# Optimization experiments

Hardware: AMD Instinct MI355X
Metric: run time of the kernel (lower is better)

The kernel has to match this reference:

```python
import jax, jax.numpy as jnp
import numpy as np

D_EMBED = 512
N_HEAD = 8
N_LAYER = 12
B, S = 4, 1024


def setup_inputs() -> dict:
    key = jax.random.key(0)
    ks = jax.random.split(key, 8)
    std = 0.02
    x = jax.random.normal(ks[0], (B, S, D_EMBED), dtype=jnp.float32)
    e = jax.random.normal(ks[1], (B, S, D_EMBED), dtype=jnp.float32)
    p = jax.random.normal(ks[2], (S, D_EMBED), dtype=jnp.float32)
    W_q = std * jax.random.normal(ks[3], (N_HEAD, D_EMBED, D_EMBED), dtype=jnp.float32)
    W_k = std * jax.random.normal(ks[4], (N_HEAD, D_EMBED, D_EMBED), dtype=jnp.float32)
    W_v = std * jax.random.normal(ks[5], (N_HEAD, D_EMBED, D_EMBED), dtype=jnp.float32)
    # torch Linear weight: (out_features, in_features) = (E, H*E)
    W_o = (std / np.sqrt(2 * N_LAYER)) * jax.random.normal(ks[6], (D_EMBED, N_HEAD * D_EMBED), dtype=jnp.float32)
    gamma = std * jax.random.normal(ks[7], (1, N_HEAD, 1, 1), dtype=jnp.float32)
    return {"x": x, "e": e, "p": p, "W_q": W_q, "W_k": W_k, "W_v": W_v, "W_o": W_o, "gamma": gamma}


def reference(x, e, p, W_q, W_k, W_v, W_o, gamma):
    # use_ppe_attn=False path: Q,K,V all from x. Per-head full-dim projections.
    Q = jnp.einsum('bse,hef->bhsf', x, W_q)  # (B,H,S,E)
    K = jnp.einsum('bse,hef->bhsf', x, W_k)
    V = jnp.einsum('bse,hef->bhsf', x, W_v)
    # rbf kernel: exp(-gamma * ||q - k||_2^2), squared distance via expansion
    q2 = jnp.sum(Q * Q, axis=-1, keepdims=True)          # (B,H,S,1)
    k2 = jnp.sum(K * K, axis=-1, keepdims=True)          # (B,H,S,1)
    qk = jnp.einsum('bhse,bhte->bhst', Q, K)             # (B,H,S,S)
    d2 = jnp.maximum(q2 + jnp.swapaxes(k2, -2, -1) - 2.0 * qk, 0.0)
    attn = jnp.exp(-gamma * d2)                          # (B,H,S,S)
    out = jnp.einsum('bhst,bhte->bhse', attn, V)         # (B,H,S,E)
    out = jnp.transpose(out, (0, 2, 1, 3)).reshape(x.shape[0], x.shape[1], -1)  # (B,S,H*E)
    return out @ W_o.T                                   # (B,S,E)
```

## Files before the change

### kernel.cpp

```cpp
#include <hip/hip_runtime.h>
#include <cstdint>
#include <cstring>

typedef unsigned short ushort_t;
typedef __attribute__((ext_vector_type(8))) short short8;
typedef __attribute__((ext_vector_type(4))) float f32x4;
typedef __attribute__((ext_vector_type(4))) unsigned short us4;

constexpr int Hh = 8;
constexpr int Ss = 1024;
constexpr int Ee = 512;

__device__ __forceinline__ ushort_t f2bf(float f) {
    uint32_t u; __builtin_memcpy(&u, &f, 4);
    u += 0x7fffu + ((u >> 16) & 1u);
    return (ushort_t)(u >> 16);
}
__device__ __forceinline__ float bf2f(ushort_t h) {
    uint32_t u = ((uint32_t)h) << 16; float f; __builtin_memcpy(&f, &u, 4); return f;
}

__device__ __forceinline__ void gload_lds16(const ushort_t* g, void* lds) {
    __builtin_amdgcn_global_load_lds(
        (const __attribute__((address_space(1))) void*)g,
        (__attribute__((address_space(3))) void*)lds, 16, 0, 0);
}


__global__ void cvt_f32_bf16(const float4* __restrict__ in, us4* __restrict__ out, int n4) {
    int i = blockIdx.x * blockDim.x + threadIdx.x;
    if (i < n4) {
        float4 v = in[i];
        us4 o = { f2bf(v.x), f2bf(v.y), f2bf(v.z), f2bf(v.w) };
        out[i] = o;
    }
}

__global__ void wtrans(const float* __restrict__ W, ushort_t* __restrict__ Wt) {
    __shared__ float tile[32][33];
    int h = blockIdx.z;
    int e0 = blockIdx.y * 32, f0 = blockIdx.x * 32;
    int tx = threadIdx.x, ty = threadIdx.y;
    #pragma unroll
    for (int i = 0; i < 4; i++) {
        int e = e0 + ty + i * 8;
        tile[ty + i * 8][tx] = W[((size_t)h * 512 + e) * 512 + f0 + tx];
    }
    __syncthreads();
    #pragma unroll
    for (int i = 0; i < 4; i++) {
        int f = f0 + ty + i * 8;
        Wt[((size_t)h * 512 + f) * 512 + e0 + tx] = f2bf(tile[tx][ty + i * 8]);
    }
}

__global__ void sumsq(const ushort_t* __restrict__ X, float* __restrict__ out) {
    int row = blockIdx.x * 4 + (threadIdx.x >> 6);
    int ln = threadIdx.x & 63;
    short8 v = *(const short8*)(X + (size_t)row * 512 + ln * 8);
    float s = 0.f;
    #pragma unroll
    for (int j = 0; j < 8; j++) {
        float f = bf2f((ushort_t)v[j]);
        s += f * f;
    }
    #pragma unroll
    for (int off = 32; off > 0; off >>= 1) s += __shfl_xor(s, off);
    if (ln == 0) out[row] = s;
}

__global__ void reduce8(const f32x4* __restrict__ p, f32x4* __restrict__ out, int n4) {
    int i = blockIdx.x * blockDim.x + threadIdx.x;
    if (i < n4) {
        f32x4 a = __builtin_nontemporal_load(p + i);
        #pragma unroll
        for (int j = 1; j < 8; j++) a += __builtin_nontemporal_load(p + i + (size_t)j * n4);
        out[i] = a;
    }
}

template<int EPI>
__global__ __launch_bounds__(512, 1)
void gemm256(const ushort_t* __restrict__ A, int lda,
             const ushort_t* __restrict__ Bm, int ldb,
             void* __restrict__ Cout, int K,
             const float* __restrict__ q2, const float* __restrict__ k2,
             const float* __restrict__ gamma, int bIdx)
{
    __shared__ __align__(16) ushort_t SMEM[65536];

    const int t  = threadIdx.x;
    const int wv = t >> 6, ln = t & 63;
    const int wm = wv >> 2, wn = wv & 3;

    const int gx = gridDim.x, gy = gridDim.y;
    const int gxy = gx * gy;
    const int L = blockIdx.x + gx * (blockIdx.y + gy * blockIdx.z);
    const int xcd = L & 7;
    const int j = L >> 3;
    const int z  = xcd + 8 * (j / gxy);
    const int rem = j % gxy;
    const int by = rem / gx;
    const int bx = rem % gx;

    const int m0 = by * 256, n0 = bx * 256;

    int bh = z;
    if constexpr (EPI == 2 || EPI == 3) bh = (bIdx < 0) ? z : (bIdx * Hh + z);

    const ushort_t* Ab = A;
    const ushort_t* Bb = Bm;
    if constexpr (EPI == 0 || EPI == 1) { Bb = Bm + (size_t)z * Ee * Ee; }
    if constexpr (EPI == 2) {
        Ab = A  + (size_t)bh * Ss * Ee;
        Bb = Bm + (size_t)bh * Ss * Ee;
    }
    if constexpr (EPI == 3) {
        Ab = A  + (size_t)z * Ss * Ss;
        Bb = Bm + (size_t)bh * Ee * Ss;
    }
    if constexpr (EPI == 4) {
        Ab = A  + (size_t)z * 512;
        Bb = Bm + (size_t)z * 512;
    }

    f32x4 acc[8][4];
    #pragma unroll
    for (int i = 0; i < 8; i++)
        #pragma unroll
        for (int j2 = 0; j2 < 4; j2++) acc[i][j2] = (f32x4){0.f, 0.f, 0.f, 0.f};

    const int srow = ln >> 3;
    const int schk = ((ln & 7) ^ srow) * 8;
    const ushort_t* sbase[4][2];
    int ldso[4][2];
    #pragma unroll
    for (int kind = 0; kind < 4; ++kind) {
        #pragma unroll
        for (int c = 0; c < 2; ++c) {
            const int idx = (kind & 1) * 16 + wv * 2 + c;
            const int rb = idx * 8 + srow;
            sbase[kind][c] = (kind < 2)
                ? Ab + (size_t)(m0 + rb) * lda + schk
                : Bb + (size_t)(n0 + rb) * ldb + schk;
            ldso[kind][c] = (kind < 2 ? 0 : 32768) + idx * 512;
        }
    }
    auto STAGE_UNIT = [&](int tile, int kind) {
        const int k0 = tile << 6;
        const int par = (tile & 1) * 16384;
        #pragma unroll
        for (int c = 0; c < 2; ++c)
            gload_lds16(sbase[kind][c] + k0, &SMEM[ldso[kind][c] + par]);
    };

    const int T = K >> 6;

    #pragma unroll
    for (int kk = 0; kk < 4; ++kk) STAGE_UNIT(0, kk);
    #pragma unroll
    for (int kk = 0; kk < 4; ++kk) STAGE_UNIT(1, kk);
    asm volatile("s_waitcnt vmcnt(8)" ::: "memory");
    __builtin_amdgcn_s_barrier();

    const int lrow = ln & 15, lkg = ln >> 4;
    const int swz = lrow & 7;

    for (int u = 0; u < (T >> 1); ++u) {
        short8 bfr[4][2];
        #pragma unroll
        for (int p = 0; p < 8; ++p) {
            const int d = p >> 2, q = p & 3;

            if (q == 0) {
                #pragma unroll
                for (int fc = 0; fc < 4; fc++)
                    #pragma unroll
                    for (int kg = 0; kg < 2; kg++)
                        bfr[fc][kg] = *(const short8*)(&SMEM[32768 + d * 16384 +
                                          (wn * 64 + fc * 16 + lrow) * 64 +
                                          (((kg * 4 + lkg) ^ swz) << 3)]);
            }
            short8 af[2][2];
            #pragma unroll
            for (int j2 = 0; j2 < 2; j2++)
                #pragma unroll
                for (int kg = 0; kg < 2; kg++)
                    af[j2][kg] = *(const short8*)(&SMEM[d * 16384 +
                                     (wm * 128 + (q * 2 + j2) * 16 + lrow) * 64 +
                                     (((kg * 4 + lkg) ^ swz) << 3)]);

            {
                int stile, skind;
                if      (p == 0) { stile = 2 * u + 1; skind = 0; }
                else if (p == 1) { stile = 2 * u + 1; skind = 1; }
                else if (p == 2) { stile = 2 * u + 2; skind = 2; }
                else if (p == 3) { stile = 2 * u + 2; skind = 3; }
                else if (p == 4) { stile = 2 * u + 2; skind = 0; }
                else if (p == 5) { stile = 2 * u + 2; skind = 1; }
                else if (p == 6) { stile = 2 * u + 3; skind = 2; }
                else             { stile = 2 * u + 3; skind = 3; }
                if (stile < T && !(u == 0 && stile == 1))
                    STAGE_UNIT(stile, skind);
            }

            __builtin_amdgcn_s_barrier();

            __builtin_amdgcn_s_setprio(1);
            #pragma unroll
            for (int j2 = 0; j2 < 2; j2++)
                #pragma unroll
                for (int fc = 0; fc < 4; fc++)
                    #pragma unroll
                    for (int kg = 0; kg < 2; kg++)
                        acc[q * 2 + j2][fc] = __builtin_amdgcn_mfma_f32_16x16x32_bf16(
                            af[j2][kg], bfr[fc][kg], acc[q * 2 + j2][fc], 0, 0, 0);
            __builtin_amdgcn_s_setprio(0);

            if (p == 3) {
                if (2 * u + 2 < T) asm volatile("s_waitcnt vmcnt(4)" ::: "memory");
                else               asm volatile("s_waitcnt vmcnt(0)" ::: "memory");
            }
            if (p == 7 && (u + 1) < (T >> 1)) {
                asm volatile("s_waitcnt vmcnt(4)" ::: "memory");
            }

            __builtin_amdgcn_s_barrier();
        }
    }

    const int crow = (ln >> 4) * 4, ccol = ln & 15;

    if constexpr (EPI == 1) {
        ushort_t* O = (ushort_t*)Cout;
        #pragma unroll
        for (int fr = 0; fr < 8; fr++) {
            #pragma unroll
            for (int fc = 0; fc < 4; fc++) {
                int gm0 = m0 + wm * 128 + fr * 16 + crow;
                int gn  = n0 + wn * 64 + fc * 16 + ccol;
                int b = gm0 >> 10, s = gm0 & 1023;
                us4 pk = { f2bf(acc[fr][fc][0]), f2bf(acc[fr][fc][1]),
                           f2bf(acc[fr][fc][2]), f2bf(acc[fr][fc][3]) };
                __builtin_nontemporal_store(pk, (us4*)(O + ((size_t)(b * Hh + z) * Ee + gn) * Ss + s));
            }
        }
    } else if constexpr (EPI == 4) {
        float* O = (float*)Cout + (size_t)z * 4096 * 512;
        float* fscr = (float*)SMEM + wv * 2176;
        for (int pass = 0; pass < 4; ++pass) {
            #pragma unroll
            for (int fr2 = 0; fr2 < 2; fr2++) {
                int fr = pass * 2 + fr2;
                #pragma unroll
                for (int fc = 0; fc < 4; fc++)
                    #pragma unroll
                    for (int i = 0; i < 4; i++)
                        fscr[(fr2 * 16 + crow + i) * 68 + fc * 16 + ccol] = acc[fr][fc][i];
            }
            #pragma unroll
            for (int rr = 0; rr < 8; ++rr) {
                int r = rr * 4 + (ln >> 4);
                int c = (ln & 15) * 4;
                f32x4 v = *(const f32x4*)&fscr[r * 68 + c];
                int gm = m0 + wm * 128 + pass * 32 + r;
                int gn = n0 + wn * 64 + c;
                __builtin_nontemporal_store(v, (f32x4*)&O[(size_t)gm * 512 + gn]);
            }
        }
    } else {
        ushort_t* scr = SMEM + wv * 4608;
        float g = 0.f; const float* q2b = nullptr; const float* k2b = nullptr;
        float k2v[4];
        if constexpr (EPI == 2) {
            g = gamma[z & 7];
            q2b = q2 + (size_t)bh * Ss;
            k2b = k2 + (size_t)bh * Ss;
            #pragma unroll
            for (int fc = 0; fc < 4; fc++) k2v[fc] = k2b[n0 + wn * 64 + fc * 16 + ccol];
        }
        for (int pass = 0; pass < 2; ++pass) {
            float q2p[4][4];
            if constexpr (EPI == 2) {
                #pragma unroll
                for (int fr2 = 0; fr2 < 4; fr2++)
                    #pragma unroll
                    for (int i = 0; i < 4; i++)
                        q2p[fr2][i] = q2b[m0 + wm * 128 + pass * 64 + fr2 * 16 + crow + i];
            }
            #pragma unroll
            for (int fr2 = 0; fr2 < 4; fr2++) {
                int fr = pass * 4 + fr2;
                #pragma unroll
                for (int fc = 0; fc < 4; fc++) {
                    #pragma unroll
                    for (int i = 0; i < 4; i++) {
                        float v = acc[fr][fc][i];
                        if constexpr (EPI == 2) {
                            float d2 = fmaxf(q2p[fr2][i] + k2v[fc] - 2.0f * v, 0.0f);
                            v = __expf(-g * d2);
                        }
                        scr[(fr2 * 16 + crow + i) * 72 + fc * 16 + ccol] = f2bf(v);
                    }
                }
            }
            #pragma unroll
            for (int rr = 0; rr < 8; ++rr) {
                int r = rr * 8 + (ln >> 3);
                int c = (ln & 7) * 8;
                short8 v = *(const short8*)&scr[r * 72 + c];
                int gm = m0 + wm * 128 + pass * 64 + r;
                int gn = n0 + wn * 64 + c;
                ushort_t* O = (ushort_t*)Cout;
                size_t addr;
                if constexpr (EPI == 0) {
                    int b = gm >> 10, s = gm & 1023;
                    addr = ((size_t)(b * Hh + z) * Ss + s) * Ee + gn;
                } else if constexpr (EPI == 2) {
                    addr = ((size_t)z * Ss + gm) * Ss + gn;
                } else {
                    int bo = (bIdx < 0) ? (z >> 3) : bIdx;
                    int hh = (bIdx < 0) ? (z & 7) : z;
                    addr = ((size_t)(bo * Ss + gm)) * (Hh * Ee) + (size_t)hh * Ee + gn;
                }
                __builtin_nontemporal_store(v, (short8*)&O[addr]);
            }
        }
    }
}


extern "C" void kernel_launch(void* const* d_in, const int* in_sizes, int n_in,
                              void* d_out, int out_size, void* d_ws, size_t ws_size,
                              hipStream_t stream)
{
    const float* x     = (const float*)d_in[0];
    const float* Wq    = (const float*)d_in[3];
    const float* Wk    = (const float*)d_in[4];
    const float* Wv    = (const float*)d_in[5];
    const float* Wo    = (const float*)d_in[6];
    const float* gamma = (const float*)d_in[7];

    char* ws = (char*)d_ws;
    size_t off = 0;
    auto alloc = [&](size_t bytes) -> void* {
        void* p = ws + off;
        off += (bytes + 255) & ~(size_t)255;
        return p;
    };
    ushort_t* xb    = (ushort_t*)alloc(4096ull * 512 * 2);
    ushort_t* WqT   = (ushort_t*)alloc(8ull * 512 * 512 * 2);
    ushort_t* WkT   = (ushort_t*)alloc(8ull * 512 * 512 * 2);
    ushort_t* WvT   = (ushort_t*)alloc(8ull * 512 * 512 * 2);
    ushort_t* WoB   = (ushort_t*)alloc(512ull * 4096 * 2);
    ushort_t* Qb    = (ushort_t*)alloc(4ull * 8 * 1024 * 512 * 2);
    ushort_t* Kb    = (ushort_t*)alloc(4ull * 8 * 1024 * 512 * 2);
    ushort_t* Vt    = (ushort_t*)alloc(4ull * 8 * 512 * 1024 * 2);
    float*    q2    = (float*)alloc(32768ull * 4);
    float*    k2    = (float*)alloc(32768ull * 4);

    size_t off_common = off;
    size_t need_merged = off_common + 64ull * 1024 * 1024;
    bool merged = (ws_size >= need_merged);

    ushort_t* attn;
    ushort_t* Ob;
    float* fpart;
    if (merged) {
        attn = (ushort_t*)alloc(32ull * 1024 * 1024 * 2);
        Ob   = Qb;
        fpart = (float*)attn;
    } else {
        attn = (ushort_t*)alloc(8ull * 1024 * 1024 * 2);
        Ob   = (ushort_t*)alloc(4096ull * 4096 * 2);
        fpart = (float*)Qb;
    }
    (void)in_sizes; (void)n_in; (void)out_size;

    cvt_f32_bf16<<<2048, 256, 0, stream>>>((const float4*)x,  (us4*)xb,  524288);
    cvt_f32_bf16<<<2048, 256, 0, stream>>>((const float4*)Wo, (us4*)WoB, 524288);

    dim3 tb(32, 8);
    wtrans<<<dim3(16, 16, 8), tb, 0, stream>>>(Wq, WqT);
    wtrans<<<dim3(16, 16, 8), tb, 0, stream>>>(Wk, WkT);
    wtrans<<<dim3(16, 16, 8), tb, 0, stream>>>(Wv, WvT);

    gemm256<0><<<dim3(2, 16, 8), 512, 0, stream>>>(xb, 512, WqT, 512, Qb, 512, nullptr, nullptr, nullptr, 0);
    gemm256<0><<<dim3(2, 16, 8), 512, 0, stream>>>(xb, 512, WkT, 512, Kb, 512, nullptr, nullptr, nullptr, 0);
    gemm256<1><<<dim3(2, 16, 8), 512, 0, stream>>>(xb, 512, WvT, 512, Vt, 512, nullptr, nullptr, nullptr, 0);

    sumsq<<<16384, 256, 0, stream>>>(Qb, q2);

    if (merged) {
        gemm256<2><<<dim3(4, 4, 32), 512, 0, stream>>>(Qb, 512, Kb, 512, attn, 512, q2, k2, gamma, -1);
        gemm256<3><<<dim3(2, 4, 32), 512, 0, stream>>>(attn, 1024, Vt, 1024, Ob, 1024, nullptr, nullptr, nullptr, -1);
    } else {
        for (int b = 0; b < 4; b++) {
            gemm256<2><<<dim3(4, 4, 8), 512, 0, stream>>>(Qb, 512, Kb, 512, attn, 512, q2, k2, gamma, b);
            gemm256<3><<<dim3(2, 4, 8), 512, 0, stream>>>(attn, 1024, Vt, 1024, Ob, 1024, nullptr, nullptr, nullptr, b);
        }
    }

    gemm256<4><<<dim3(2, 16, 8), 512, 0, stream>>>(Ob, 4096, WoB, 4096, fpart, 512, nullptr, nullptr, nullptr, 0);
    reduce8<<<2048, 256, 0, stream>>>((const f32x4*)fpart, (f32x4*)d_out, 524288);
}
```

Before: 244.2 us.

## Batch QKV projections into one launch and cut output split-K from 8 to 2

```diff
diff --git a/kernel.cpp b/kernel.cpp
--- a/kernel.cpp
+++ b/kernel.cpp
@@ -36,9 +36,12 @@
     }
 }
 
-__global__ void wtrans(const float* __restrict__ W, ushort_t* __restrict__ Wt) {
+__global__ void wtrans_all(const float* __restrict__ Wq, const float* __restrict__ Wk,
+                           const float* __restrict__ Wv, ushort_t* __restrict__ Wt) {
     __shared__ float tile[32][33];
-    int h = blockIdx.z;
+    int zz = blockIdx.z;
+    int h = zz & 7, sel = zz >> 3;
+    const float* W = (sel == 0 ? Wq : (sel == 1 ? Wk : Wv));
     int e0 = blockIdx.y * 32, f0 = blockIdx.x * 32;
     int tx = threadIdx.x, ty = threadIdx.y;
     #pragma unroll
@@ -50,7 +53,7 @@
     #pragma unroll
     for (int i = 0; i < 4; i++) {
         int f = f0 + ty + i * 8;
-        Wt[((size_t)h * 512 + f) * 512 + e0 + tx] = f2bf(tile[tx][ty + i * 8]);
+        Wt[((size_t)zz * 512 + f) * 512 + e0 + tx] = f2bf(tile[tx][ty + i * 8]);
     }
 }
 
@@ -69,23 +72,19 @@
     if (ln == 0) out[row] = s;
 }
 
-__global__ void reduce8(const f32x4* __restrict__ p, f32x4* __restrict__ out, int n4) {
+__global__ void reduce2(const f32x4* __restrict__ p, f32x4* __restrict__ out, int n4) {
     int i = blockIdx.x * blockDim.x + threadIdx.x;
-    if (i < n4) {
-        f32x4 a = __builtin_nontemporal_load(p + i);
-        #pragma unroll
-        for (int j = 1; j < 8; j++) a += __builtin_nontemporal_load(p + i + (size_t)j * n4);
-        out[i] = a;
-    }
+    if (i < n4) out[i] = p[i] + p[i + (size_t)n4];
 }
 
 template<int EPI>
-__global__ __launch_bounds__(512, 1)
-void gemm256(const ushort_t* __restrict__ A, int lda,
-             const ushort_t* __restrict__ Bm, int ldb,
-             void* __restrict__ Cout, int K,
-             const float* __restrict__ q2, const float* __restrict__ k2,
-             const float* __restrict__ gamma, int bIdx)
+__device__ __forceinline__
+void gemm256_body(const ushort_t* __restrict__ A, int lda,
+                  const ushort_t* __restrict__ Bm, int ldb,
+                  void* __restrict__ Cout, int K,
+                  const float* __restrict__ q2, const float* __restrict__ k2,
+                  const float* __restrict__ gamma, int bIdx,
+                  void* __restrict__ Cout2)
 {
     __shared__ __align__(16) ushort_t SMEM[65536];
 
@@ -110,7 +109,7 @@
 
     const ushort_t* Ab = A;
     const ushort_t* Bb = Bm;
-    if constexpr (EPI == 0 || EPI == 1) { Bb = Bm + (size_t)z * Ee * Ee; }
+    if constexpr (EPI == 5) { Bb = Bm + (size_t)z * Ee * Ee; }
     if constexpr (EPI == 2) {
         Ab = A  + (size_t)bh * Ss * Ee;
         Bb = Bm + (size_t)bh * Ss * Ee;
@@ -118,10 +117,6 @@
     if constexpr (EPI == 3) {
         Ab = A  + (size_t)z * Ss * Ss;
         Bb = Bm + (size_t)bh * Ee * Ss;
-    }
-    if constexpr (EPI == 4) {
-        Ab = A  + (size_t)z * 512;
-        Bb = Bm + (size_t)z * 512;
     }
 
     f32x4 acc[8][4];
@@ -231,8 +226,12 @@
 
     const int crow = (ln >> 4) * 4, ccol = ln & 15;
 
-    if constexpr (EPI == 1) {
-        ushort_t* O = (ushort_t*)Cout;
+    bool vtpath = false;
+    if constexpr (EPI == 5) vtpath = ((z >> 3) == 2);
+
+    if (vtpath) {
+        ushort_t* O = (ushort_t*)Cout2;
+        const int h = z & 7;
         #pragma unroll
         for (int fr = 0; fr < 8; fr++) {
             #pragma unroll
@@ -242,30 +241,7 @@
                 int b = gm0 >> 10, s = gm0 & 1023;
                 us4 pk = { f2bf(acc[fr][fc][0]), f2bf(acc[fr][fc][1]),
                            f2bf(acc[fr][fc][2]), f2bf(acc[fr][fc][3]) };
-                __builtin_nontemporal_store(pk, (us4*)(O + ((size_t)(b * Hh + z) * Ee + gn) * Ss + s));
-            }
-        }
-    } else if constexpr (EPI == 4) {
-        float* O = (float*)Cout + (size_t)z * 4096 * 512;
-        float* fscr = (float*)SMEM + wv * 2176;
-        for (int pass = 0; pass < 4; ++pass) {
-            #pragma unroll
-            for (int fr2 = 0; fr2 < 2; fr2++) {
-                int fr = pass * 2 + fr2;
-                #pragma unroll
-                for (int fc = 0; fc < 4; fc++)
-                    #pragma unroll
-                    for (int i = 0; i < 4; i++)
-                        fscr[(fr2 * 16 + crow + i) * 68 + fc * 16 + ccol] = acc[fr][fc][i];
-            }
-            #pragma unroll
-            for (int rr = 0; rr < 8; ++rr) {
-                int r = rr * 4 + (ln >> 4);
-                int c = (ln & 15) * 4;
-                f32x4 v = *(const f32x4*)&fscr[r * 68 + c];
-                int gm = m0 + wm * 128 + pass * 32 + r;
-                int gn = n0 + wn * 64 + c;
-                __builtin_nontemporal_store(v, (f32x4*)&O[(size_t)gm * 512 + gn]);
+                *(us4*)(O + ((size_t)(b * Hh + h) * Ee + gn) * Ss + s) = pk;
             }
         }
     } else {
@@ -313,9 +289,10 @@
                 int gn = n0 + wn * 64 + c;
                 ushort_t* O = (ushort_t*)Cout;
                 size_t addr;
-                if constexpr (EPI == 0) {
+                if constexpr (EPI == 5) {
+                    int mat = z >> 3, h = z & 7;
                     int b = gm >> 10, s = gm & 1023;
-                    addr = ((size_t)(b * Hh + z) * Ss + s) * Ee + gn;
+                    addr = (size_t)mat * 16777216 + ((size_t)(b * Hh + h) * Ss + s) * Ee + gn;
                 } else if constexpr (EPI == 2) {
                     addr = ((size_t)z * Ss + gm) * Ss + gn;
                 } else {
@@ -323,8 +300,115 @@
                     int hh = (bIdx < 0) ? (z & 7) : z;
                     addr = ((size_t)(bo * Ss + gm)) * (Hh * Ee) + (size_t)hh * Ee + gn;
                 }
-                __builtin_nontemporal_store(v, (short8*)&O[addr]);
-            }
+                *(short8*)&O[addr] = v;
+            }
+        }
+    }
+}
+
+__global__ __launch_bounds__(512, 1)
+void g_proj(const ushort_t* A, int lda, const ushort_t* Bm, int ldb, void* C, int K,
+            const float* q2, const float* k2, const float* gamma, int bIdx, void* C2)
+{ gemm256_body<5>(A, lda, Bm, ldb, C, K, q2, k2, gamma, bIdx, C2); }
+
+__global__ __launch_bounds__(512, 1)
+void g_scores(const ushort_t* A, int lda, const ushort_t* Bm, int ldb, void* C, int K,
+              const float* q2, const float* k2, const float* gamma, int bIdx, void* C2)
+{ gemm256_body<2>(A, lda, Bm, ldb, C, K, q2, k2, gamma, bIdx, C2); }
+
+__global__ __launch_bounds__(512, 1)
+void g_pv(const ushort_t* A, int lda, const ushort_t* Bm, int ldb, void* C, int K,
+          const float* q2, const float* k2, const float* gamma, int bIdx, void* C2)
+{ gemm256_body<3>(A, lda, Bm, ldb, C, K, q2, k2, gamma, bIdx, C2); }
+
+__global__ __launch_bounds__(256)
+void g_final(const ushort_t* __restrict__ A, int lda,
+             const ushort_t* __restrict__ Bm, int ldb,
+             float* __restrict__ Cout, int K)
+{
+    __shared__ __align__(16) ushort_t SMEM[16384];
+
+    const int t  = threadIdx.x;
+    const int wv = t >> 6, ln = t & 63;
+    const int wr = wv >> 1, wc = wv & 1;
+
+    const int gx = gridDim.x, gy = gridDim.y;
+    const int nwg = gx * gy * gridDim.z;
+    const int L = blockIdx.x + gx * (blockIdx.y + gy * blockIdx.z);
+    const int wid = (L & 7) * (nwg >> 3) + (L >> 3);
+    const int bx = wid % gx;
+    const int tmp = wid / gx;
+    const int by = tmp % gy;
+    const int z  = tmp / gy;
+
+    const int m0 = by * 128, n0 = bx * 128;
+    const ushort_t* Ab = A  + (size_t)z * 2048;
+    const ushort_t* Bb = Bm + (size_t)z * 2048;
+
+    f32x4 acc[4][4];
+    #pragma unroll
+    for (int i = 0; i < 4; i++)
+        #pragma unroll
+        for (int j = 0; j < 4; j++) acc[i][j] = (f32x4){0.f, 0.f, 0.f, 0.f};
+
+    const int rstage = t >> 2;
+    const int cchunk = t & 3;
+
+    auto STAGE = [&](int ti, int buf) {
+        const int k0 = ti << 5;
+        #pragma unroll
+        for (int i = 0; i < 2; i++) {
+            gload_lds16(Ab + (size_t)(m0 + i * 64 + rstage) * lda + k0 + cchunk * 8,
+                        (char*)SMEM + buf * 8192 + i * 4096 + wv * 1024);
+            gload_lds16(Bb + (size_t)(n0 + i * 64 + rstage) * ldb + k0 + cchunk * 8,
+                        (char*)SMEM + 16384 + buf * 8192 + i * 4096 + wv * 1024);
+        }
+    };
+
+    const int nt = K >> 5;
+    STAGE(0, 0);
+    __syncthreads();
+
+    int cur = 0;
+    const int lrow = ln & 15, kg = ln >> 4;
+    for (int ti = 0; ti < nt; ++ti) {
+        if (ti + 1 < nt) STAGE(ti + 1, cur ^ 1);
+
+        short8 af[4], bfr[4];
+        #pragma unroll
+        for (int fr = 0; fr < 4; fr++)
+            af[fr] = *(const short8*)(&SMEM[cur * 4096 + (wr * 64 + fr * 16 + lrow) * 32 + kg * 8]);
+        #pragma unroll
+        for (int fc = 0; fc < 4; fc++)
+            bfr[fc] = *(const short8*)(&SMEM[8192 + cur * 4096 + (wc * 64 + fc * 16 + lrow) * 32 + kg * 8]);
+        #pragma unroll
+        for (int fr = 0; fr < 4; fr++)
+            #pragma unroll
+            for (int fc = 0; fc < 4; fc++)
+                acc[fr][fc] = __builtin_amdgcn_mfma_f32_16x16x32_bf16(af[fr], bfr[fc], acc[fr][fc], 0, 0, 0);
+
+        __syncthreads();
+        cur ^= 1;
+    }
+
+    const int crow = (ln >> 4) * 4, ccol = ln & 15;
+    float* O = Cout + (size_t)z * 4096 * 512;
+    float* fscr = (float*)SMEM + wv * 1088;
+    #pragma unroll
+    for (int pass = 0; pass < 4; ++pass) {
+        #pragma unroll
+        for (int fc = 0; fc < 4; fc++)
+            #pragma unroll
+            for (int i = 0; i < 4; i++)
+                fscr[(crow + i) * 68 + fc * 16 + ccol] = acc[pass][fc][i];
+        #pragma unroll
+        for (int rr = 0; rr < 4; ++rr) {
+            int r = rr * 4 + (ln >> 4);
+            int c = (ln & 15) * 4;
+            f32x4 v = *(const f32x4*)&fscr[r * 68 + c];
+            int gm = m0 + wr * 64 + pass * 16 + r;
+            int gn = n0 + wc * 64 + c;
+            *(f32x4*)&O[(size_t)gm * 512 + gn] = v;
         }
     }
 }
@@ -349,9 +433,7 @@
         return p;
     };
     ushort_t* xb    = (ushort_t*)alloc(4096ull * 512 * 2);
-    ushort_t* WqT   = (ushort_t*)alloc(8ull * 512 * 512 * 2);
-    ushort_t* WkT   = (ushort_t*)alloc(8ull * 512 * 512 * 2);
-    ushort_t* WvT   = (ushort_t*)alloc(8ull * 512 * 512 * 2);
+    ushort_t* Wt    = (ushort_t*)alloc(24ull * 512 * 512 * 2);
     ushort_t* WoB   = (ushort_t*)alloc(512ull * 4096 * 2);
     ushort_t* Qb    = (ushort_t*)alloc(4ull * 8 * 1024 * 512 * 2);
     ushort_t* Kb    = (ushort_t*)alloc(4ull * 8 * 1024 * 512 * 2);
@@ -381,26 +463,23 @@
     cvt_f32_bf16<<<2048, 256, 0, stream>>>((const float4*)Wo, (us4*)WoB, 524288);
 
     dim3 tb(32, 8);
-    wtrans<<<dim3(16, 16, 8), tb, 0, stream>>>(Wq, WqT);
-    wtrans<<<dim3(16, 16, 8), tb, 0, stream>>>(Wk, WkT);
-    wtrans<<<dim3(16, 16, 8), tb, 0, stream>>>(Wv, WvT);
-
-    gemm256<0><<<dim3(2, 16, 8), 512, 0, stream>>>(xb, 512, WqT, 512, Qb, 512, nullptr, nullptr, nullptr, 0);
-    gemm256<0><<<dim3(2, 16, 8), 512, 0, stream>>>(xb, 512, WkT, 512, Kb, 512, nullptr, nullptr, nullptr, 0);
-    gemm256<1><<<dim3(2, 16, 8), 512, 0, stream>>>(xb, 512, WvT, 512, Vt, 512, nullptr, nullptr, nullptr, 0);
+    wtrans_all<<<dim3(16, 16, 24), tb, 0, stream>>>(Wq, Wk, Wv, Wt);
+
+    g_proj<<<dim3(2, 16, 24), 512, 0, stream>>>(xb, 512, Wt, 512, Qb, 512,
+                                                nullptr, nullptr, nullptr, 0, Vt);
 
     sumsq<<<16384, 256, 0, stream>>>(Qb, q2);
 
     if (merged) {
-        gemm256<2><<<dim3(4, 4, 32), 512, 0, stream>>>(Qb, 512, Kb, 512, attn, 512, q2, k2, gamma, -1);
-        gemm256<3><<<dim3(2, 4, 32), 512, 0, stream>>>(attn, 1024, Vt, 1024, Ob, 1024, nullptr, nullptr, nullptr, -1);
+        g_scores<<<dim3(4, 4, 32), 512, 0, stream>>>(Qb, 512, Kb, 512, attn, 512, q2, k2, gamma, -1, nullptr);
+        g_pv<<<dim3(2, 4, 32), 512, 0, stream>>>(attn, 1024, Vt, 1024, Ob, 1024, nullptr, nullptr, nullptr, -1, nullptr);
     } else {
         for (int b = 0; b < 4; b++) {
-            gemm256<2><<<dim3(4, 4, 8), 512, 0, stream>>>(Qb, 512, Kb, 512, attn, 512, q2, k2, gamma, b);
-            gemm256<3><<<dim3(2, 4, 8), 512, 0, stream>>>(attn, 1024, Vt, 1024, Ob, 1024, nullptr, nullptr, nullptr, b);
-        }
-    }
-
-    gemm256<4><<<dim3(2, 16, 8), 512, 0, stream>>>(Ob, 4096, WoB, 4096, fpart, 512, nullptr, nullptr, nullptr, 0);
-    reduce8<<<2048, 256, 0, stream>>>((const f32x4*)fpart, (f32x4*)d_out, 524288);
-}
+            g_scores<<<dim3(4, 4, 8), 512, 0, stream>>>(Qb, 512, Kb, 512, attn, 512, q2, k2, gamma, b, nullptr);
+            g_pv<<<dim3(2, 4, 8), 512, 0, stream>>>(attn, 1024, Vt, 1024, Ob, 1024, nullptr, nullptr, nullptr, b, nullptr);
+        }
+    }
+
+    g_final<<<dim3(4, 32, 2), 256, 0, stream>>>(Ob, 4096, WoB, 4096, fpart, 2048);
+    reduce2<<<2048, 256, 0, stream>>>((const f32x4*)fpart, (f32x4*)d_out, 524288);
+}
```

Result: faster. 213.5 us (median of 3 runs) (-12.5%).
